# Performance work log

Hardware: AMD Instinct MI355X
Metric: run time of the kernel (lower is better)

The kernel has to match this reference:

```python
import jax, jax.numpy as jnp
import numpy as np

WH, WW = 7, 7
N = WH * WW
DIM = 384
HEADS = 12
NW = 64          # windows per image
B_ = 2048        # batch * NW


def _relative_position_index():
    ch, cw = np.meshgrid(np.arange(WH), np.arange(WW), indexing='ij')
    coords = np.stack([ch, cw]).reshape(2, -1)                      # [2, N]
    rel = coords[:, :, None] - coords[:, None, :]                   # [2, N, N]
    rel = rel.transpose(1, 2, 0)
    rel[:, :, 0] += WH - 1
    rel[:, :, 1] += WW - 1
    rel[:, :, 0] *= 2 * WW - 1
    return jnp.asarray(rel.sum(-1), dtype=jnp.int32)                # [N, N]


def setup_inputs() -> dict:
    key = jax.random.key(0)
    ks = jax.random.split(key, 7)
    return {
        'x': jax.random.normal(ks[0], (B_, N, DIM), dtype=jnp.float32),
        'qkv_w': jax.random.normal(ks[1], (3 * DIM, DIM), dtype=jnp.float32) * 0.02,
        'qkv_b': jax.random.normal(ks[2], (3 * DIM,), dtype=jnp.float32) * 0.02,
        'proj_w': jax.random.normal(ks[3], (DIM, DIM), dtype=jnp.float32) * 0.02,
        'proj_b': jax.random.normal(ks[4], (DIM,), dtype=jnp.float32) * 0.02,
        'bias_table': jax.random.normal(ks[5], ((2 * WH - 1) * (2 * WW - 1), HEADS), dtype=jnp.float32) * 0.02,
        'mask': jax.random.normal(ks[6], (NW, N, N), dtype=jnp.float32),
        'rel_idx': _relative_position_index(),
    }


def reference(x, qkv_w, qkv_b, proj_w, proj_b, bias_table, mask, rel_idx):
    B_, n, C = x.shape
    H = HEADS
    hd = C // H
    scale = hd ** (-0.5)

    qkv = x @ qkv_w.T + qkv_b                                        # [B_, N, 3C]
    qkv = qkv.reshape(B_, n, 3, H, hd).transpose(2, 0, 3, 1, 4)      # [3, B_, H, N, hd]
    q, k, v = qkv[0], qkv[1], qkv[2]

    attn = jnp.einsum('bhqd,bhkd->bhqk', q * scale, k)               # [B_, H, N, N]

    rpb = bias_table[rel_idx.reshape(-1)].reshape(n, n, H)           # gather [N, N, H]
    attn = attn + rpb.transpose(2, 0, 1)[None]                       # [B_, H, N, N]

    nW = mask.shape[0]
    attn = attn.reshape(B_ // nW, nW, H, n, n) + mask[None, :, None]
    attn = attn.reshape(B_, H, n, n)
    attn = jax.nn.softmax(attn, axis=-1)

    out = jnp.einsum('bhqk,bhkd->bhqd', attn, v)                     # [B_, H, N, hd]
    out = out.transpose(0, 2, 1, 3).reshape(B_, n, C)
    return out @ proj_w.T + proj_b
```

## Files before the change

### kernel.cpp

```cpp
#include <hip/hip_runtime.h>
#include <hip/hip_bf16.h>
#include <cstdint>
#include <cstddef>

#define NTOK 49
#define DIM 384
#define KDIM 384
#define HEADS 12
#define HD 32
#define BATCH 2048
#define MROWS (BATCH * NTOK)

typedef unsigned short u16;
typedef __bf16 bf16x8 __attribute__((ext_vector_type(8)));
typedef unsigned short u16x8 __attribute__((ext_vector_type(8)));
typedef float f32x4 __attribute__((ext_vector_type(4)));
typedef float f32x16 __attribute__((ext_vector_type(16)));

__device__ __forceinline__ u16 f2b(float f) {
  union { float f; unsigned u; } v; v.f = f;
  unsigned r = v.u + 0x7fffu + ((v.u >> 16) & 1u);
  return (u16)(r >> 16);
}

__device__ __forceinline__ bf16x8 ld_bf8(const u16* p) {
  u16x8 u = *(const u16x8*)p;
  return __builtin_bit_cast(bf16x8, u);
}

__device__ __forceinline__ void gload_lds16(const void* g, void* l) {
  __builtin_amdgcn_global_load_lds(
      (const __attribute__((address_space(1))) unsigned*)g,
      (__attribute__((address_space(3))) unsigned*)l, 16, 0, 0);
}

__device__ __forceinline__ unsigned pkbf(float lo, float hi) {
  unsigned r;
  asm("v_cvt_pk_bf16_f32 %0, %1, %2" : "=v"(r) : "v"(lo), "v"(hi));
  return r;
}

__global__ __launch_bounds__(256) void k_prep(const float* __restrict__ x,
                                              u16* __restrict__ xb,
                                              const float* __restrict__ qkv_w,
                                              u16* __restrict__ wqkvb,
                                              const float* __restrict__ proj_w,
                                              u16* __restrict__ wprojb,
                                              const float* __restrict__ bias_table,
                                              const float* __restrict__ mask,
                                              const int* __restrict__ rel_idx,
                                              float* __restrict__ rpbm) {
  int blk = blockIdx.x;
  if (blk < 38208) {
    const float* in;
    u16* out;
    int i;
    if (blk < 37632) {
      in = x; out = xb; i = blk * 256 + threadIdx.x;
    } else if (blk < 38064) {
      in = qkv_w; out = wqkvb; i = (blk - 37632) * 256 + threadIdx.x;
    } else {
      in = proj_w; out = wprojb; i = (blk - 38064) * 256 + threadIdx.x;
    }
    float4 v = ((const float4*)in)[i];
    ushort4 o;
    o.x = f2b(v.x); o.y = f2b(v.y); o.z = f2b(v.z); o.w = f2b(v.w);
    ((ushort4*)out)[i] = o;
  } else {
    int gidx = (blk - 38208) * 256 + threadIdx.x;
    int l    = gidx & 63;
    int rq   = (gidx >> 6) & 3;
    int tile = (gidx >> 8) & 3;
    int w    = (gidx >> 10) & 63;
    int h    = gidx >> 16;
    int mi = tile >> 1, nj = tile & 1;
    int kk0 = mi * 32 + 8 * rq + 4 * (l >> 5);
    int qq  = nj * 32 + (l & 31);
    float4 out;
    float* op = (float*)&out;
#pragma unroll
    for (int rl = 0; rl < 4; ++rl) {
      int kk = kk0 + rl;
      float v = -1e30f;
      if (kk < NTOK && qq < NTOK)
        v = bias_table[rel_idx[qq * NTOK + kk] * HEADS + h] +
            mask[(w * NTOK + qq) * NTOK + kk];
      op[rl] = v;
    }
    ((float4*)rpbm)[gidx] = out;
  }
}

template <int OUT_BF16, int NCOLS, int NTN, int GD8>
__global__ __launch_bounds__(512, 4) void k_gemm256(const u16* __restrict__ A,
                                                    const u16* __restrict__ B,
                                                    const float* __restrict__ bias,
                                                    void* __restrict__ Cv) {
  __shared__ u16 sh[36864];
  int bid = blockIdx.x;
  int tile = (bid & 7) * GD8 + (bid >> 3);
  int mt = tile / NTN, nt = tile - mt * NTN;
  long m0 = (long)mt * 256;
  int n0 = nt * 128;
  int tid = threadIdx.x;
  int lane = tid & 63, wid = tid >> 6;
  int wr = (wid >> 1) * 64, wc = (wid & 1) * 64;
  int c = lane & 15, g = lane >> 4;
  int gsw = (g ^ ((c >> 1) & 3)) * 8;

  int srow = wid * 16 + (lane >> 2);
  int scol = ((lane & 3) ^ ((lane >> 3) & 3)) * 8;
  const u16* gA = A + (m0 + srow) * (long)KDIM + scol;
  const u16* gB = B + (long)(n0 + srow) * KDIM + scol;
  int lrow = srow, lseg = (lane & 3) * 8;

  f32x4 acc[4][4] = {};
  bf16x8 af[4], bfr[4];

#define STAGE256(BUF, KT)                                                      \
  {                                                                            \
    u16* As_ = sh + (BUF) * 12288;                                             \
    u16* Bs_ = As_ + 8192;                                                     \
    gload_lds16(gA + (KT), &As_[lrow * 32 + lseg]);                            \
    gload_lds16(gA + (KT) + 128L * KDIM, &As_[(lrow + 128) * 32 + lseg]);      \
    gload_lds16(gB + (KT), &Bs_[lrow * 32 + lseg]);                            \
  }

#define FRAGREAD(BUF)                                                          \
  {                                                                            \
    const u16* As = sh + (BUF) * 12288;                                        \
    const u16* Bs = As + 8192;                                                 \
    _Pragma("unroll") for (int i = 0; i < 4; ++i) {                            \
      af[i]  = ld_bf8(&As[(wr + i * 16 + c) * 32 + gsw]);                      \
      bfr[i] = ld_bf8(&Bs[(wc + i * 16 + c) * 32 + gsw]);                      \
    }                                                                          \
  }

#define MFMA_CL                                                                \
  __builtin_amdgcn_s_setprio(1);                                               \
  _Pragma("unroll") for (int mi = 0; mi < 4; ++mi)                             \
  _Pragma("unroll") for (int ni = 0; ni < 4; ++ni)                             \
      acc[mi][ni] = __builtin_amdgcn_mfma_f32_16x16x32_bf16(                   \
          af[mi], bfr[ni], acc[mi][ni], 0, 0, 0);                              \
  __builtin_amdgcn_s_setprio(0);

#define GITER(T, NV)                                                           \
  {                                                                            \
    MFMA_CL;                                                                   \
    asm volatile("s_waitcnt vmcnt(" #NV ")" ::: "memory");                     \
    __builtin_amdgcn_s_barrier();                                              \
    __builtin_amdgcn_sched_barrier(0);                                         \
    if ((T) + 3 < 12) STAGE256((T) % 3, ((T) + 3) * 32);                       \
    FRAGREAD(((T) + 1) % 3);                                                   \
  }

  STAGE256(0, 0);
  STAGE256(1, 32);
  STAGE256(2, 64);
  asm volatile("s_waitcnt vmcnt(6)" ::: "memory");
  __builtin_amdgcn_s_barrier();
  __builtin_amdgcn_sched_barrier(0);
  FRAGREAD(0);

  GITER(0, 3)  GITER(1, 3)  GITER(2, 3)  GITER(3, 3)
  GITER(4, 3)  GITER(5, 3)  GITER(6, 3)  GITER(7, 3)
  GITER(8, 3)  GITER(9, 3)  GITER(10, 0)
  { MFMA_CL; }
  __builtin_amdgcn_s_barrier();
#undef GITER
#undef MFMA_CL
#undef FRAGREAD
#undef STAGE256

  if (OUT_BF16) {
    u16* C = (u16*)Cv;
#pragma unroll
    for (int mi = 0; mi < 4; ++mi)
#pragma unroll
      for (int ni = 0; ni < 4; ++ni) {
        int col = wc + ni * 16 + c;
        float bv = bias[n0 + col];
#pragma unroll
        for (int r = 0; r < 4; ++r) {
          int row = wr + mi * 16 + g * 4 + r;
          sh[row * 128 + col] = f2b(acc[mi][ni][r] + bv);
        }
      }
    __syncthreads();
#pragma unroll
    for (int rep = 0; rep < 8; ++rep) {
      int idx = rep * 4096 + tid * 8;
      int row = idx >> 7, col = idx & 127;
      int grow = (int)m0 + row;
      int b = grow / 49, tok = grow - b * 49;
      int gcol = n0 + col;
      int t = gcol / 384;
      int hc = gcol - t * 384;
      int h = hc >> 5, d0 = hc & 31;
      size_t off = (((size_t)(t * 12 + h) * BATCH + b) * 49 + tok) * 32 + d0;
      *(u16x8*)(C + off) = *(const u16x8*)&sh[idx];
    }
  } else {
    float* C = (float*)Cv;
    float* shf = (float*)sh;
#pragma unroll
    for (int chunk = 0; chunk < 2; ++chunk) {
      __syncthreads();
      if ((wid >> 2) == chunk) {
#pragma unroll
        for (int mi = 0; mi < 4; ++mi)
#pragma unroll
          for (int ni = 0; ni < 4; ++ni) {
            int col = wc + ni * 16 + c;
            float bv = bias[n0 + col];
#pragma unroll
            for (int r = 0; r < 4; ++r) {
              int lr = ((wid >> 1) & 1) * 64 + mi * 16 + g * 4 + r;
              shf[lr * 128 + col] = acc[mi][ni][r] + bv;
            }
          }
      }
      __syncthreads();
#pragma unroll
      for (int rep = 0; rep < 8; ++rep) {
        int idx = rep * 2048 + tid * 4;
        int row = idx >> 7, col = idx & 127;
        *(float4*)(C + (m0 + chunk * 128 + row) * NCOLS + n0 + col) =
            *(const float4*)&shf[idx];
      }
    }
  }
}

__global__ __launch_bounds__(256, 4) void k_attn(const u16* __restrict__ qkv,
                                                 const float* __restrict__ rpbmT,
                                                 u16* __restrict__ attnout) {
  int lane = threadIdx.x & 63, wid = threadIdx.x >> 6;
  int blk0 = blockIdx.x;
  int blk = (blk0 & 7) * 768 + (blk0 >> 3);
  int w = blk / 96;
  int rr = blk - w * 96;
  int j = rr / 3;
  int hb = rr - j * 3;
  int b = j * 64 + w;
  int h = hb * 4 + wid;
  int l31 = lane & 31, hi = lane >> 5;

  const u16* qh = qkv + ((size_t)(h)*BATCH + b) * (49 * 32);
  const u16* kh = qkv + ((size_t)(12 + h) * BATCH + b) * (49 * 32);
  const u16* vh = qkv + ((size_t)(24 + h) * BATCH + b) * (49 * 32);

  bf16x8 kf[2][2], qf[2][2];
#pragma unroll
  for (int mi = 0; mi < 2; ++mi) {
    int row = mi * 32 + l31; if (row > NTOK - 1) row = NTOK - 1;
#pragma unroll
    for (int k2 = 0; k2 < 2; ++k2)
      kf[mi][k2] = ld_bf8(kh + row * 32 + k2 * 16 + hi * 8);
  }
#pragma unroll
  for (int nj = 0; nj < 2; ++nj) {
    int row = nj * 32 + l31; if (row > NTOK - 1) row = NTOK - 1;
#pragma unroll
    for (int k2 = 0; k2 < 2; ++k2)
      qf[nj][k2] = ld_bf8(qh + row * 32 + k2 * 16 + hi * 8);
  }

  f32x16 s[2][2];
  f32x16 z16 = {};
  __builtin_amdgcn_s_setprio(1);
#pragma unroll
  for (int mi = 0; mi < 2; ++mi)
#pragma unroll
    for (int nj = 0; nj < 2; ++nj) {
      s[mi][nj] = __builtin_amdgcn_mfma_f32_32x32x16_bf16(kf[mi][0], qf[nj][0],
                                                          z16, 0, 0, 0);
      s[mi][nj] = __builtin_amdgcn_mfma_f32_32x32x16_bf16(kf[mi][1], qf[nj][1],
                                                          s[mi][nj], 0, 0, 0);
    }
  __builtin_amdgcn_s_setprio(0);

  const float scale = 0.17677669529663687f;
  const f32x4* rp = (const f32x4*)(rpbmT + ((size_t)(h * 64 + w)) * 4096);
#pragma unroll
  for (int mi = 0; mi < 2; ++mi)
#pragma unroll
    for (int nj = 0; nj < 2; ++nj)
#pragma unroll
      for (int rq = 0; rq < 4; ++rq) {
        f32x4 rv = rp[(mi * 2 + nj) * 256 + rq * 64 + lane];
#pragma unroll
        for (int rl = 0; rl < 4; ++rl)
          s[mi][nj][rq * 4 + rl] = s[mi][nj][rq * 4 + rl] * scale + rv[rl];
      }

#pragma unroll
  for (int nj = 0; nj < 2; ++nj) {
    float mx = s[0][nj][0];
#pragma unroll
    for (int mi = 0; mi < 2; ++mi)
#pragma unroll
      for (int r = 0; r < 16; ++r)
        mx = fmaxf(mx, s[mi][nj][r]);
    mx = fmaxf(mx, __shfl_xor(mx, 32));
    float sum = 0.f;
#pragma unroll
    for (int mi = 0; mi < 2; ++mi)
#pragma unroll
      for (int r = 0; r < 16; ++r) {
        float p = __expf(s[mi][nj][r] - mx);
        s[mi][nj][r] = p;
        sum += p;
      }
    sum += __shfl_xor(sum, 32);
    float inv = __builtin_amdgcn_rcpf(sum);
#pragma unroll
    for (int mi = 0; mi < 2; ++mi)
#pragma unroll
      for (int r = 0; r < 16; ++r)
        s[mi][nj][r] *= inv;
  }

  f32x16 o[2] = {};
#pragma unroll
  for (int kk = 0; kk < 4; ++kk) {
    u16x8 tmp;
#pragma unroll
    for (int e = 0; e < 8; ++e)
      tmp[e] = vh[(kk * 16 + hi * 8 + e) * 32 + l31];
    bf16x8 vbk = __builtin_bit_cast(bf16x8, tmp);
    __builtin_amdgcn_s_setprio(1);
#pragma unroll
    for (int nj = 0; nj < 2; ++nj) {
      const int mi = kk >> 1, br = (kk & 1) * 8;
      unsigned t0 = pkbf(s[mi][nj][br + 0], s[mi][nj][br + 1]);
      unsigned t1 = pkbf(s[mi][nj][br + 2], s[mi][nj][br + 3]);
      unsigned t2 = pkbf(s[mi][nj][br + 4], s[mi][nj][br + 5]);
      unsigned t3 = pkbf(s[mi][nj][br + 6], s[mi][nj][br + 7]);
      asm("v_permlane32_swap_b32 %0, %1" : "+v"(t0), "+v"(t2));
      asm("v_permlane32_swap_b32 %0, %1" : "+v"(t1), "+v"(t3));
      uint4 uu; uu.x = t0; uu.y = t1; uu.z = t2; uu.w = t3;
      bf16x8 pa = __builtin_bit_cast(bf16x8, uu);
      o[nj] = __builtin_amdgcn_mfma_f32_32x32x16_bf16(pa, vbk, o[nj], 0, 0, 0);
    }
    __builtin_amdgcn_s_setprio(0);
  }

  u16* obase = attnout + (size_t)b * (NTOK * DIM) + h * HD;
#pragma unroll
  for (int nj = 0; nj < 2; ++nj)
#pragma unroll
    for (int r = 0; r < 16; ++r) {
      int q = nj * 32 + (r & 3) + 8 * (r >> 2) + 4 * hi;
      if (q < NTOK)
        obase[(size_t)q * DIM + l31] = f2b(o[nj][r]);
    }
}

extern "C" void kernel_launch(void* const* d_in, const int* in_sizes, int n_in,
                              void* d_out, int out_size, void* d_ws, size_t ws_size,
                              hipStream_t stream) {
  const float* x       = (const float*)d_in[0];
  const float* qkv_w   = (const float*)d_in[1];
  const float* qkv_b   = (const float*)d_in[2];
  const float* proj_w  = (const float*)d_in[3];
  const float* proj_b  = (const float*)d_in[4];
  const float* bias_tb = (const float*)d_in[5];
  const float* mask    = (const float*)d_in[6];
  const int*   rel_idx = (const int*)d_in[7];
  float* out = (float*)d_out;

  char* ws = (char*)d_ws;
  u16*   xb      = (u16*)(ws + 0);
  u16*   wqkvb   = (u16*)(ws + 77070336);
  u16*   wprojb  = (u16*)(ws + 77955072);
  float* rpbm    = (float*)(ws + 78249984);
  u16*   qkv     = (u16*)(ws + 90832896);
  u16*   attnout = (u16*)(ws + 322043904);

  k_prep<<<41280, 256, 0, stream>>>(x, xb, qkv_w, wqkvb, proj_w, wprojb,
                                    bias_tb, mask, rel_idx, rpbm);

  k_gemm256<1, 1152, 9, 441><<<3528, 512, 0, stream>>>(xb, wqkvb, qkv_b,
                                                       (void*)qkv);

  k_attn<<<6144, 256, 0, stream>>>(qkv, rpbm, attnout);

  k_gemm256<0, 384, 3, 147><<<1176, 512, 0, stream>>>(attnout, wprojb, proj_b,
                                                      (void*)out);

  (void)in_sizes; (void)n_in; (void)out_size; (void)ws_size;
}
```

Before: 335.9 us.

## Move bias-mask table build into QKV GEMM launch and prefetch V in attention

The relative-position-bias plus mask table construction moves out of the prep kernel and into extra leading blocks of the QKV GEMM launch. Those blocks return early, so the table build can overlap with GEMM tiles instead of sitting on the elementwise prep path. In the attention kernel, all V fragments are loaded up front before the QK MFMA so their latency is hidden, and the occupancy hint drops from 4 to 3 blocks to allow more registers. The risks are that the GEMM blocks, which carry a large LDS allocation, now also run the table build, and that the attention kernel has lower occupancy.

```diff
diff --git a/kernel.cpp b/kernel.cpp
--- a/kernel.cpp
+++ b/kernel.cpp
@@ -45,29 +45,37 @@
                                               const float* __restrict__ qkv_w,
                                               u16* __restrict__ wqkvb,
                                               const float* __restrict__ proj_w,
-                                              u16* __restrict__ wprojb,
-                                              const float* __restrict__ bias_table,
-                                              const float* __restrict__ mask,
-                                              const int* __restrict__ rel_idx,
-                                              float* __restrict__ rpbm) {
+                                              u16* __restrict__ wprojb) {
   int blk = blockIdx.x;
-  if (blk < 38208) {
-    const float* in;
-    u16* out;
-    int i;
-    if (blk < 37632) {
-      in = x; out = xb; i = blk * 256 + threadIdx.x;
-    } else if (blk < 38064) {
-      in = qkv_w; out = wqkvb; i = (blk - 37632) * 256 + threadIdx.x;
-    } else {
-      in = proj_w; out = wprojb; i = (blk - 38064) * 256 + threadIdx.x;
-    }
-    float4 v = ((const float4*)in)[i];
-    ushort4 o;
-    o.x = f2b(v.x); o.y = f2b(v.y); o.z = f2b(v.z); o.w = f2b(v.w);
-    ((ushort4*)out)[i] = o;
+  const float* in;
+  u16* out;
+  int i;
+  if (blk < 37632) {
+    in = x; out = xb; i = blk * 256 + threadIdx.x;
+  } else if (blk < 38064) {
+    in = qkv_w; out = wqkvb; i = (blk - 37632) * 256 + threadIdx.x;
   } else {
-    int gidx = (blk - 38208) * 256 + threadIdx.x;
+    in = proj_w; out = wprojb; i = (blk - 38064) * 256 + threadIdx.x;
+  }
+  float4 v = ((const float4*)in)[i];
+  ushort4 o;
+  o.x = f2b(v.x); o.y = f2b(v.y); o.z = f2b(v.z); o.w = f2b(v.w);
+  ((ushort4*)out)[i] = o;
+}
+
+template <int OUT_BF16, int NCOLS, int NTN, int GD8, int RB>
+__global__ __launch_bounds__(512, 4) void k_gemm256(const u16* __restrict__ A,
+                                                    const u16* __restrict__ B,
+                                                    const float* __restrict__ bias,
+                                                    void* __restrict__ Cv,
+                                                    const float* __restrict__ bias_table,
+                                                    const float* __restrict__ mask,
+                                                    const int* __restrict__ rel_idx,
+                                                    float* __restrict__ rpbm) {
+  __shared__ u16 sh[36864];
+  int bid = blockIdx.x;
+  if (RB > 0 && bid < RB) {
+    int gidx = bid * 512 + threadIdx.x;
     int l    = gidx & 63;
     int rq   = (gidx >> 6) & 3;
     int tile = (gidx >> 8) & 3;
@@ -88,16 +96,9 @@
       op[rl] = v;
     }
     ((float4*)rpbm)[gidx] = out;
-  }
-}
-
-template <int OUT_BF16, int NCOLS, int NTN, int GD8>
-__global__ __launch_bounds__(512, 4) void k_gemm256(const u16* __restrict__ A,
-                                                    const u16* __restrict__ B,
-                                                    const float* __restrict__ bias,
-                                                    void* __restrict__ Cv) {
-  __shared__ u16 sh[36864];
-  int bid = blockIdx.x;
+    return;
+  }
+  bid -= RB;
   int tile = (bid & 7) * GD8 + (bid >> 3);
   int mt = tile / NTN, nt = tile - mt * NTN;
   long m0 = (long)mt * 256;
@@ -232,7 +233,7 @@
   }
 }
 
-__global__ __launch_bounds__(256, 4) void k_attn(const u16* __restrict__ qkv,
+__global__ __launch_bounds__(256, 3) void k_attn(const u16* __restrict__ qkv,
                                                  const float* __restrict__ rpbmT,
                                                  u16* __restrict__ attnout) {
   int lane = threadIdx.x & 63, wid = threadIdx.x >> 6;
@@ -266,6 +267,16 @@
       qf[nj][k2] = ld_bf8(qh + row * 32 + k2 * 16 + hi * 8);
   }
 
+  bf16x8 vb[4];
+#pragma unroll
+  for (int kk = 0; kk < 4; ++kk) {
+    u16x8 tmp;
+#pragma unroll
+    for (int e = 0; e < 8; ++e)
+      tmp[e] = vh[(kk * 16 + hi * 8 + e) * 32 + l31];
+    vb[kk] = __builtin_bit_cast(bf16x8, tmp);
+  }
+
   f32x16 s[2][2];
   f32x16 z16 = {};
   __builtin_amdgcn_s_setprio(1);
@@ -324,11 +335,6 @@
   f32x16 o[2] = {};
 #pragma unroll
   for (int kk = 0; kk < 4; ++kk) {
-    u16x8 tmp;
-#pragma unroll
-    for (int e = 0; e < 8; ++e)
-      tmp[e] = vh[(kk * 16 + hi * 8 + e) * 32 + l31];
-    bf16x8 vbk = __builtin_bit_cast(bf16x8, tmp);
     __builtin_amdgcn_s_setprio(1);
 #pragma unroll
     for (int nj = 0; nj < 2; ++nj) {
@@ -341,7 +347,7 @@
       asm("v_permlane32_swap_b32 %0, %1" : "+v"(t1), "+v"(t3));
       uint4 uu; uu.x = t0; uu.y = t1; uu.z = t2; uu.w = t3;
       bf16x8 pa = __builtin_bit_cast(bf16x8, uu);
-      o[nj] = __builtin_amdgcn_mfma_f32_32x32x16_bf16(pa, vbk, o[nj], 0, 0, 0);
+      o[nj] = __builtin_amdgcn_mfma_f32_32x32x16_bf16(pa, vb[kk], o[nj], 0, 0, 0);
     }
     __builtin_amdgcn_s_setprio(0);
   }
@@ -378,16 +384,15 @@
   u16*   qkv     = (u16*)(ws + 90832896);
   u16*   attnout = (u16*)(ws + 322043904);
 
-  k_prep<<<41280, 256, 0, stream>>>(x, xb, qkv_w, wqkvb, proj_w, wprojb,
-                                    bias_tb, mask, rel_idx, rpbm);
-
-  k_gemm256<1, 1152, 9, 441><<<3528, 512, 0, stream>>>(xb, wqkvb, qkv_b,
-                                                       (void*)qkv);
+  k_prep<<<38208, 256, 0, stream>>>(x, xb, qkv_w, wqkvb, proj_w, wprojb);
+
+  k_gemm256<1, 1152, 9, 441, 1536><<<5064, 512, 0, stream>>>(
+      xb, wqkvb, qkv_b, (void*)qkv, bias_tb, mask, rel_idx, rpbm);
 
   k_attn<<<6144, 256, 0, stream>>>(qkv, rpbm, attnout);
 
-  k_gemm256<0, 384, 3, 147><<<1176, 512, 0, stream>>>(attnout, wprojb, proj_b,
-                                                      (void*)out);
+  k_gemm256<0, 384, 3, 147, 0><<<1176, 512, 0, stream>>>(
+      attnout, wprojb, proj_b, (void*)out, nullptr, nullptr, nullptr, nullptr);
 
   (void)in_sizes; (void)n_in; (void)out_size; (void)ws_size;
 }
```

New measurement: 355.9 us. 1.06x slower.
